# Kernel optimization log

Hardware: AMD Instinct MI355X
Metric: run time of the kernel (lower is better)

Reference implementation:

```python
import jax, jax.numpy as jnp
import numpy as np

B, T, E = 2, 2048, 1024
H = 16            # num_heads (global in source repo)
D = E // H        # head_len
LN_EPS = 1e-5


def setup_inputs() -> dict:
    key = jax.random.key(0)
    ks = jax.random.split(key, 12)
    s = lambda fan_in: 1.0 / np.sqrt(fan_in)
    return {
        "x":     jax.random.normal(ks[0], (B, T, E), jnp.float32),
        "ln1_g": jnp.ones((E,), jnp.float32),
        "ln1_b": jnp.zeros((E,), jnp.float32),
        "Wq":    jax.random.normal(ks[1], (E, E), jnp.float32) * s(E),
        "Wk":    jax.random.normal(ks[2], (E, E), jnp.float32) * s(E),
        "Wv":    jax.random.normal(ks[3], (E, E), jnp.float32) * s(E),
        "Wo":    jax.random.normal(ks[4], (E, E), jnp.float32) * s(E),
        "bo":    jnp.zeros((E,), jnp.float32),
        "ln2_g": jnp.ones((E,), jnp.float32),
        "ln2_b": jnp.zeros((E,), jnp.float32),
        "W1":    jax.random.normal(ks[5], (E, 4 * E), jnp.float32) * s(E),
        "b1":    jnp.zeros((4 * E,), jnp.float32),
        "W2":    jax.random.normal(ks[6], (4 * E, E), jnp.float32) * s(4 * E),
        "b2":    jnp.zeros((E,), jnp.float32),
    }


def _layernorm(x, g, b):
    mu = jnp.mean(x, axis=-1, keepdims=True)
    var = jnp.mean(jnp.square(x - mu), axis=-1, keepdims=True)
    return (x - mu) * jax.lax.rsqrt(var + LN_EPS) * g + b


def _attention(x, Wq, Wk, Wv, Wo, bo):
    b, t, e = x.shape
    q = (x @ Wq).reshape(b, t, H, D)
    k = (x @ Wk).reshape(b, t, H, D)
    v = (x @ Wv).reshape(b, t, H, D)
    scores = jnp.einsum("bqhd,bkhd->bhqk", q, k) / np.sqrt(D).astype(np.float32)
    causal = jnp.tril(jnp.ones((t, t), bool))
    scores = jnp.where(causal, scores, -jnp.inf)
    attn = jax.nn.softmax(scores, axis=-1)
    out = jnp.einsum("bhqk,bkhd->bqhd", attn, v).reshape(b, t, e)
    return out @ Wo + bo


def reference(x, ln1_g, ln1_b, Wq, Wk, Wv, Wo, bo, ln2_g, ln2_b, W1, b1, W2, b2):
    # pre-norm attention + residual (dropout=0 / eval mode)
    x = x + _attention(_layernorm(x, ln1_g, ln1_b), Wq, Wk, Wv, Wo, bo)
    # pre-norm MLP + residual
    h = _layernorm(x, ln2_g, ln2_b)
    h = jax.nn.relu(h @ W1 + b1) @ W2 + b2
    return x + h
```

## Files before the change

kernel.cpp:

```cpp
#include <hip/hip_runtime.h>
#include <cmath>
#include <cstdint>
#include <cstddef>

typedef __bf16 bf16_t;
typedef __bf16 bf16x8 __attribute__((ext_vector_type(8)));
typedef float  f32x4  __attribute__((ext_vector_type(4)));

#define B_   2
#define T_   2048
#define E_   1024
#define H_   16
#define D_   64
#define FF_  4096
#define NROW (B_ * T_)
#define QS_  (3 * E_)
#define NTI  (T_ / 64)

__global__ __launch_bounds__(256) void ln_kernel(
    const float* __restrict__ x, const float* __restrict__ g,
    const float* __restrict__ bta, bf16_t* __restrict__ out)
{
    int row = blockIdx.x;
    int tid = threadIdx.x;
    const float4* xr = (const float4*)(x + (size_t)row * E_);
    float4 v = xr[tid];
    float s  = v.x + v.y + v.z + v.w;
    float ss = v.x * v.x + v.y * v.y + v.z * v.z + v.w * v.w;
#pragma unroll
    for (int off = 32; off; off >>= 1) {
        s  += __shfl_xor(s, off);
        ss += __shfl_xor(ss, off);
    }
    __shared__ float red[8];
    int wave = tid >> 6, lane = tid & 63;
    if (lane == 0) { red[wave] = s; red[4 + wave] = ss; }
    __syncthreads();
    s  = red[0] + red[1] + red[2] + red[3];
    ss = red[4] + red[5] + red[6] + red[7];
    float mu   = s * (1.0f / E_);
    float var  = ss * (1.0f / E_) - mu * mu;
    float rstd = rsqrtf(var + 1e-5f);
    float4 gv = ((const float4*)g)[tid];
    float4 bv = ((const float4*)bta)[tid];
    union { bf16_t h[4]; ushort4 u; } pk;
    pk.h[0] = (bf16_t)((v.x - mu) * rstd * gv.x + bv.x);
    pk.h[1] = (bf16_t)((v.y - mu) * rstd * gv.y + bv.y);
    pk.h[2] = (bf16_t)((v.z - mu) * rstd * gv.z + bv.z);
    pk.h[3] = (bf16_t)((v.w - mu) * rstd * gv.w + bv.w);
    ((ushort4*)(out + (size_t)row * E_))[tid] = pk.u;
}

__global__ __launch_bounds__(256) void ln_reduce2(
    const float* __restrict__ p, const float* __restrict__ bias,
    const float* __restrict__ resid, float* __restrict__ x1,
    const float* __restrict__ g, const float* __restrict__ bta,
    bf16_t* __restrict__ out)
{
    int row = blockIdx.x;
    int tid = threadIdx.x;
    size_t off = (size_t)row * E_;
    float4 v0 = ((const float4*)(p + off))[tid];
    float4 v1 = ((const float4*)(p + (size_t)NROW * E_ + off))[tid];
    float4 bb = ((const float4*)bias)[tid];
    float4 rr = ((const float4*)(resid + off))[tid];
    float4 v;
    v.x = v0.x + v1.x + bb.x + rr.x;
    v.y = v0.y + v1.y + bb.y + rr.y;
    v.z = v0.z + v1.z + bb.z + rr.z;
    v.w = v0.w + v1.w + bb.w + rr.w;
    ((float4*)(x1 + off))[tid] = v;
    float s  = v.x + v.y + v.z + v.w;
    float ss = v.x * v.x + v.y * v.y + v.z * v.z + v.w * v.w;
#pragma unroll
    for (int o = 32; o; o >>= 1) {
        s  += __shfl_xor(s, o);
        ss += __shfl_xor(ss, o);
    }
    __shared__ float red[8];
    int wave = tid >> 6, lane = tid & 63;
    if (lane == 0) { red[wave] = s; red[4 + wave] = ss; }
    __syncthreads();
    s  = red[0] + red[1] + red[2] + red[3];
    ss = red[4] + red[5] + red[6] + red[7];
    float mu   = s * (1.0f / E_);
    float var  = ss * (1.0f / E_) - mu * mu;
    float rstd = rsqrtf(var + 1e-5f);
    float4 gv = ((const float4*)g)[tid];
    float4 bv = ((const float4*)bta)[tid];
    union { bf16_t h[4]; ushort4 u; } pk;
    pk.h[0] = (bf16_t)((v.x - mu) * rstd * gv.x + bv.x);
    pk.h[1] = (bf16_t)((v.y - mu) * rstd * gv.y + bv.y);
    pk.h[2] = (bf16_t)((v.z - mu) * rstd * gv.z + bv.z);
    pk.h[3] = (bf16_t)((v.w - mu) * rstd * gv.w + bv.w);
    ((ushort4*)(out + off))[tid] = pk.u;
}

__global__ __launch_bounds__(256) void add_reduce2(
    const float* __restrict__ p, const float* __restrict__ bias,
    const float* __restrict__ resid, float* __restrict__ out)
{
    int row = blockIdx.x;
    int tid = threadIdx.x;
    size_t off = (size_t)row * E_;
    float4 v0 = ((const float4*)(p + off))[tid];
    float4 v1 = ((const float4*)(p + (size_t)NROW * E_ + off))[tid];
    float4 bb = ((const float4*)bias)[tid];
    float4 rr = ((const float4*)(resid + off))[tid];
    float4 v;
    v.x = v0.x + v1.x + bb.x + rr.x;
    v.y = v0.y + v1.y + bb.y + rr.y;
    v.z = v0.z + v1.z + bb.z + rr.z;
    v.w = v0.w + v1.w + bb.w + rr.w;
    ((float4*)(out + off))[tid] = v;
}

__global__ __launch_bounds__(256) void transpose_all(
    const float* __restrict__ Wq, const float* __restrict__ Wk,
    const float* __restrict__ Wv, const float* __restrict__ Wo,
    const float* __restrict__ W1, const float* __restrict__ W2,
    bf16_t* __restrict__ wqkv, bf16_t* __restrict__ wot,
    bf16_t* __restrict__ w1t, bf16_t* __restrict__ w2t)
{
    int l = blockIdx.x;
    const float* W; bf16_t* Wt; int K, N, bx, by;
    if (l < 4096) {
        int seg = l >> 10, r = l & 1023;
        K = E_; N = E_; bx = r & 31; by = r >> 5;
        if      (seg == 0) { W = Wq; Wt = wqkv; }
        else if (seg == 1) { W = Wk; Wt = wqkv + (size_t)E_ * E_; }
        else if (seg == 2) { W = Wv; Wt = wqkv + (size_t)2 * E_ * E_; }
        else               { W = Wo; Wt = wot; }
    } else if (l < 8192) {
        int r = l - 4096; K = E_; N = FF_; bx = r & 127; by = r >> 7;
        W = W1; Wt = w1t;
    } else {
        int r = l - 8192; K = FF_; N = E_; bx = r & 31; by = r >> 5;
        W = W2; Wt = w2t;
    }
    __shared__ float t[32][33];
    int n0 = bx * 32, k0 = by * 32;
    int tx = threadIdx.x & 31, ty = threadIdx.x >> 5;
#pragma unroll
    for (int i = 0; i < 4; ++i)
        t[ty + i * 8][tx] = W[(size_t)(k0 + ty + i * 8) * N + n0 + tx];
    __syncthreads();
#pragma unroll
    for (int i = 0; i < 4; ++i)
        Wt[(size_t)(n0 + ty + i * 8) * K + k0 + tx] = (bf16_t)t[tx][ty + i * 8];
}

#define BM 128
#define BN 128
#define BK 32

__global__ __launch_bounds__(256) void gemm_bt(
    const bf16_t* __restrict__ A, const bf16_t* __restrict__ Bt,
    const float* __restrict__ bias, const float* __restrict__ resid,
    void* __restrict__ Cout, bf16_t* __restrict__ vt_out,
    int M, int N, int K, int lda, int ldb,
    int has_bias, int do_relu, int has_resid, int out_bf16)
{
    __shared__ __attribute__((aligned(16))) bf16_t As[2][BM * BK];
    __shared__ __attribute__((aligned(16))) bf16_t Bs[2][BN * BK];
    int tid  = threadIdx.x;
    int lane = tid & 63, wave = tid >> 6;
    int m0 = blockIdx.x * BM, n0 = blockIdx.y * BN;
    int wm = (wave & 1) * 64, wn = (wave >> 1) * 64;
    int koff = blockIdx.z * K;
    f32x4 acc[4][4];
#pragma unroll
    for (int i = 0; i < 4; ++i)
#pragma unroll
        for (int j = 0; j < 4; ++j) acc[i][j] = (f32x4){0.f, 0.f, 0.f, 0.f};

    int sr = tid >> 2;
    int sc = (tid & 3) * 8;
    const int kq = (lane >> 4) * 8;
    const int ml = lane & 15;
    const bf16_t* Ag = A  + (size_t)(m0 + sr) * lda + koff + sc;
    const bf16_t* Bg = Bt + (size_t)(n0 + sr) * ldb + koff + sc;
    int niter = K / BK;

    {
        uint4 ra0 = *(const uint4*)Ag;
        uint4 ra1 = *(const uint4*)(Ag + (size_t)64 * lda);
        uint4 rb0 = *(const uint4*)Bg;
        uint4 rb1 = *(const uint4*)(Bg + (size_t)64 * ldb);
        *(uint4*)&As[0][sr * BK + sc]        = ra0;
        *(uint4*)&As[0][(sr + 64) * BK + sc] = ra1;
        *(uint4*)&Bs[0][sr * BK + sc]        = rb0;
        *(uint4*)&Bs[0][(sr + 64) * BK + sc] = rb1;
    }

    for (int it = 0; it < niter; ++it) {
        int cur = it & 1, nxt = cur ^ 1;
        __syncthreads();

        uint4 ra0, ra1, rb0, rb1;
        bool pf = (it + 1 < niter);
        if (pf) {
            int k0 = (it + 1) * BK;
            ra0 = *(const uint4*)(Ag + k0);
            ra1 = *(const uint4*)(Ag + k0 + (size_t)64 * lda);
            rb0 = *(const uint4*)(Bg + k0);
            rb1 = *(const uint4*)(Bg + k0 + (size_t)64 * ldb);
        }

        bf16x8 af[4], bfr[4];
#pragma unroll
        for (int mi = 0; mi < 4; ++mi)
            af[mi] = *(const bf16x8*)&As[cur][(wm + mi * 16 + ml) * BK + kq];
#pragma unroll
        for (int ni = 0; ni < 4; ++ni)
            bfr[ni] = *(const bf16x8*)&Bs[cur][(wn + ni * 16 + ml) * BK + kq];
#pragma unroll
        for (int mi = 0; mi < 4; ++mi)
#pragma unroll
            for (int ni = 0; ni < 4; ++ni)
                acc[mi][ni] = __builtin_amdgcn_mfma_f32_16x16x32_bf16(
                    af[mi], bfr[ni], acc[mi][ni], 0, 0, 0);

        if (pf) {
            *(uint4*)&As[nxt][sr * BK + sc]        = ra0;
            *(uint4*)&As[nxt][(sr + 64) * BK + sc] = ra1;
            *(uint4*)&Bs[nxt][sr * BK + sc]        = rb0;
            *(uint4*)&Bs[nxt][(sr + 64) * BK + sc] = rb1;
        }
    }

    int r4 = (lane >> 4) * 4;
    if (gridDim.z > 1) {
        float* P = (float*)Cout + (size_t)blockIdx.z * M * N;
#pragma unroll
        for (int mi = 0; mi < 4; ++mi)
#pragma unroll
            for (int ni = 0; ni < 4; ++ni) {
                int col = n0 + wn + ni * 16 + ml;
#pragma unroll
                for (int r = 0; r < 4; ++r) {
                    int row = m0 + wm + mi * 16 + r4 + r;
                    P[(size_t)row * N + col] = acc[mi][ni][r];
                }
            }
        return;
    }
    if (vt_out && n0 >= 2 * E_) {
#pragma unroll
        for (int mi = 0; mi < 4; ++mi)
#pragma unroll
            for (int ni = 0; ni < 4; ++ni) {
                int vcol = n0 + wn + ni * 16 + ml - 2 * E_;
                int h = vcol >> 6, d = vcol & 63;
                int row0 = m0 + wm + mi * 16 + r4;
                int b = row0 >> 11, t = row0 & (T_ - 1);
                union { bf16_t h4[4]; uint2 u; } pk;
#pragma unroll
                for (int r = 0; r < 4; ++r) pk.h4[r] = (bf16_t)acc[mi][ni][r];
                *(uint2*)&vt_out[((size_t)(b * H_ + h) * D_ + d) * T_ + t] = pk.u;
            }
        return;
    }
#pragma unroll
    for (int mi = 0; mi < 4; ++mi) {
#pragma unroll
        for (int ni = 0; ni < 4; ++ni) {
            int col = n0 + wn + ni * 16 + ml;
            float bval = has_bias ? bias[col] : 0.0f;
#pragma unroll
            for (int r = 0; r < 4; ++r) {
                int row = m0 + wm + mi * 16 + r4 + r;
                float v = acc[mi][ni][r] + bval;
                if (do_relu)   v = fmaxf(v, 0.0f);
                if (has_resid) v += resid[(size_t)row * N + col];
                if (out_bf16)
                    ((bf16_t*)Cout)[(size_t)row * N + col] = (bf16_t)v;
                else
                    ((float*)Cout)[(size_t)row * N + col] = v;
            }
        }
    }
}

#define PSTR 72

struct TileState {
    f32x4 acc[4];
    float m1, l1;
};

__device__ __forceinline__ void tile_update(
    const bf16x8 kf[2][4], const bf16x8 vf[2][4], const bf16x8 qf[2],
    TileState& st, bf16_t* PsW, int ml, int r4, int kq8,
    bool diag, int ch, int qrow)
{
    f32x4 s[4];
#pragma unroll
    for (int nt = 0; nt < 4; ++nt) {
        s[nt] = (f32x4){0.f, 0.f, 0.f, 0.f};
#pragma unroll
        for (int ks = 0; ks < 2; ++ks)
            s[nt] = __builtin_amdgcn_mfma_f32_16x16x32_bf16(kf[ks][nt], qf[ks], s[nt], 0, 0, 0);
    }
    if (diag) {
#pragma unroll
        for (int nt = 0; nt < 4; ++nt)
#pragma unroll
            for (int r = 0; r < 4; ++r)
                if (ch * 64 + nt * 16 + r4 + r > qrow) s[nt][r] = -INFINITY;
    }
    float mx = -INFINITY;
#pragma unroll
    for (int nt = 0; nt < 4; ++nt)
#pragma unroll
        for (int r = 0; r < 4; ++r) mx = fmaxf(mx, s[nt][r]);
    mx = fmaxf(mx, __shfl_xor(mx, 16));
    mx = fmaxf(mx, __shfl_xor(mx, 32));
    float mn = fmaxf(st.m1, mx);
    float al = __expf(st.m1 - mn);
    st.m1 = mn;
    float sum = 0.f;
#pragma unroll
    for (int nt = 0; nt < 4; ++nt)
#pragma unroll
        for (int r = 0; r < 4; ++r) {
            float p = __expf(s[nt][r] - mn);
            s[nt][r] = p;
            sum += p;
        }
    sum += __shfl_xor(sum, 16);
    sum += __shfl_xor(sum, 32);
    st.l1 = st.l1 * al + sum;
#pragma unroll
    for (int dt = 0; dt < 4; ++dt)
#pragma unroll
        for (int r = 0; r < 4; ++r) st.acc[dt][r] *= al;

#pragma unroll
    for (int nt = 0; nt < 4; ++nt) {
        union { bf16_t h[4]; uint2 u; } pk;
#pragma unroll
        for (int r = 0; r < 4; ++r) pk.h[r] = (bf16_t)s[nt][r];
        *(uint2*)&PsW[ml * PSTR + nt * 16 + r4] = pk.u;
    }
#pragma unroll
    for (int ks = 0; ks < 2; ++ks) {
        bf16x8 pf = *(const bf16x8*)&PsW[ml * PSTR + ks * 32 + kq8];
#pragma unroll
        for (int dt = 0; dt < 4; ++dt)
            st.acc[dt] = __builtin_amdgcn_mfma_f32_16x16x32_bf16(vf[ks][dt], pf, st.acc[dt], 0, 0, 0);
    }
}

__global__ __launch_bounds__(256) void attn_mfma(
    const bf16_t* __restrict__ Qp, const bf16_t* __restrict__ Kp,
    const bf16_t* __restrict__ Vt, bf16_t* __restrict__ O)
{
    __shared__ __attribute__((aligned(16))) bf16_t Ks[2][64 * PSTR];
    __shared__ __attribute__((aligned(16))) bf16_t Vts[2][64 * PSTR];
    __shared__ __attribute__((aligned(16))) bf16_t Ps[4][16 * PSTR];

    int tid = threadIdx.x, lane = tid & 63, wave = tid >> 6;
    int ml  = lane & 15;
    int kq8 = (lane >> 4) * 8;
    int r4  = (lane >> 4) * 4;
    int bh = blockIdx.y, b = bh >> 4, h = bh & 15;
    size_t qk_base = (size_t)b * T_ * QS_ + h * D_;
    size_t vt_base = (size_t)bh * D_ * T_;
    size_t o_base  = (size_t)b * T_ * E_ + h * D_;

    int lo = blockIdx.x, hi = NTI - 1 - blockIdx.x;
    int qlo = lo * 64 + wave * 16;
    int qhi = hi * 64 + wave * 16;

    bf16x8 qfl[2], qfh[2];
#pragma unroll
    for (int ks = 0; ks < 2; ++ks) {
        bf16x8 a = *(const bf16x8*)&Qp[qk_base + (size_t)(qlo + ml) * QS_ + ks * 32 + kq8];
        bf16x8 c = *(const bf16x8*)&Qp[qk_base + (size_t)(qhi + ml) * QS_ + ks * 32 + kq8];
#pragma unroll
        for (int j = 0; j < 8; ++j) {
            a[j] = (bf16_t)((float)a[j] * 0.125f);
            c[j] = (bf16_t)((float)c[j] * 0.125f);
        }
        qfl[ks] = a; qfh[ks] = c;
    }

    TileState stl, sth;
#pragma unroll
    for (int dt = 0; dt < 4; ++dt) {
        stl.acc[dt] = (f32x4){0.f, 0.f, 0.f, 0.f};
        sth.acc[dt] = (f32x4){0.f, 0.f, 0.f, 0.f};
    }
    stl.m1 = -INFINITY; stl.l1 = 0.f;
    sth.m1 = -INFINITY; sth.l1 = 0.f;

    int r0 = tid >> 3, c0 = (tid & 7) * 8;
    int nch = hi + 1;

    {
        const bf16_t* kb = &Kp[qk_base + (size_t)r0 * QS_ + c0];
        const bf16_t* vb = &Vt[vt_base + (size_t)r0 * T_ + c0];
        uint4 k0v = *(const uint4*)kb;
        uint4 k1v = *(const uint4*)(kb + (size_t)32 * QS_);
        uint4 v0v = *(const uint4*)vb;
        uint4 v1v = *(const uint4*)(vb + (size_t)32 * T_);
        *(uint4*)&Ks[0][r0 * PSTR + c0]         = k0v;
        *(uint4*)&Ks[0][(r0 + 32) * PSTR + c0]  = k1v;
        *(uint4*)&Vts[0][r0 * PSTR + c0]        = v0v;
        *(uint4*)&Vts[0][(r0 + 32) * PSTR + c0] = v1v;
    }

    for (int ch = 0; ch < nch; ++ch) {
        int cur = ch & 1, nxt = cur ^ 1;
        __syncthreads();

        uint4 nk0, nk1, nv0, nv1;
        bool pf = (ch + 1 < nch);
        if (pf) {
            const bf16_t* kb = &Kp[qk_base + (size_t)((ch + 1) * 64 + r0) * QS_ + c0];
            const bf16_t* vb = &Vt[vt_base + (size_t)r0 * T_ + (ch + 1) * 64 + c0];
            nk0 = *(const uint4*)kb;
            nk1 = *(const uint4*)(kb + (size_t)32 * QS_);
            nv0 = *(const uint4*)vb;
            nv1 = *(const uint4*)(vb + (size_t)32 * T_);
        }

        bf16x8 kf[2][4], vf[2][4];
#pragma unroll
        for (int ks = 0; ks < 2; ++ks)
#pragma unroll
            for (int nt = 0; nt < 4; ++nt) {
                kf[ks][nt] = *(const bf16x8*)&Ks[cur][(nt * 16 + ml) * PSTR + ks * 32 + kq8];
                vf[ks][nt] = *(const bf16x8*)&Vts[cur][(nt * 16 + ml) * PSTR + ks * 32 + kq8];
            }

        tile_update(kf, vf, qfh, sth, Ps[wave], ml, r4, kq8,
                    ch == hi, ch, qhi + ml);
        if (ch <= lo)
            tile_update(kf, vf, qfl, stl, Ps[wave], ml, r4, kq8,
                        ch == lo, ch, qlo + ml);

        if (pf) {
            *(uint4*)&Ks[nxt][r0 * PSTR + c0]         = nk0;
            *(uint4*)&Ks[nxt][(r0 + 32) * PSTR + c0]  = nk1;
            *(uint4*)&Vts[nxt][r0 * PSTR + c0]        = nv0;
            *(uint4*)&Vts[nxt][(r0 + 32) * PSTR + c0] = nv1;
        }
    }

#pragma unroll
    for (int t = 0; t < 2; ++t) {
        TileState& st = t ? stl : sth;
        int qw = t ? qlo : qhi;
        float inv = 1.0f / st.l1;
#pragma unroll
        for (int dt = 0; dt < 4; ++dt) {
            union { bf16_t h[4]; uint2 u; } pk;
#pragma unroll
            for (int r = 0; r < 4; ++r) pk.h[r] = (bf16_t)(st.acc[dt][r] * inv);
            *(uint2*)&Ps[wave][ml * PSTR + dt * 16 + r4] = pk.u;
        }
        int row = lane >> 2, seg = (lane & 3) * 16;
        bf16x8 o0 = *(const bf16x8*)&Ps[wave][row * PSTR + seg];
        bf16x8 o1 = *(const bf16x8*)&Ps[wave][row * PSTR + seg + 8];
        size_t gp = o_base + (size_t)(qw + row) * E_ + seg;
        *(bf16x8*)&O[gp]     = o0;
        *(bf16x8*)&O[gp + 8] = o1;
    }
}

extern "C" void kernel_launch(void* const* d_in, const int* in_sizes, int n_in,
                              void* d_out, int out_size, void* d_ws, size_t ws_size,
                              hipStream_t stream)
{
    const float* x    = (const float*)d_in[0];
    const float* ln1g = (const float*)d_in[1];
    const float* ln1b = (const float*)d_in[2];
    const float* Wq   = (const float*)d_in[3];
    const float* Wk   = (const float*)d_in[4];
    const float* Wv   = (const float*)d_in[5];
    const float* Wo   = (const float*)d_in[6];
    const float* bo   = (const float*)d_in[7];
    const float* ln2g = (const float*)d_in[8];
    const float* ln2b = (const float*)d_in[9];
    const float* W1   = (const float*)d_in[10];
    const float* b1   = (const float*)d_in[11];
    const float* W2   = (const float*)d_in[12];
    const float* b2   = (const float*)d_in[13];

    char* ws = (char*)d_ws;
    const size_t MB = 1024ull * 1024ull;
    bf16_t* wqkv = (bf16_t*)(ws + 0 * MB);
    bf16_t* wot  = (bf16_t*)(ws + 6 * MB);
    bf16_t* w1t  = (bf16_t*)(ws + 8 * MB);
    bf16_t* w2t  = (bf16_t*)(ws + 16 * MB);
    bf16_t* xn   = (bf16_t*)(ws + 24 * MB);
    bf16_t* QKV  = (bf16_t*)(ws + 32 * MB);
    bf16_t* att  = (bf16_t*)(ws + 56 * MB);
    float*  x1   = (float*)(ws + 64 * MB);
    bf16_t* hb   = (bf16_t*)(ws + 80 * MB);
    bf16_t* h1   = (bf16_t*)(ws + 88 * MB);
    bf16_t* Vtb  = (bf16_t*)(ws + 88 * MB);
    float*  part = (float*)(ws + 24 * MB);

    dim3 blk(256);

    transpose_all<<<dim3(12288), blk, 0, stream>>>(
        Wq, Wk, Wv, Wo, W1, W2, wqkv, wot, w1t, w2t);

    ln_kernel<<<dim3(NROW), blk, 0, stream>>>(x, ln1g, ln1b, xn);

    gemm_bt<<<dim3(NROW / BM, QS_ / BN), blk, 0, stream>>>(
        xn, wqkv, nullptr, nullptr, QKV, Vtb, NROW, QS_, E_, E_, E_, 0, 0, 0, 1);

    attn_mfma<<<dim3(NTI / 2, B_ * H_), blk, 0, stream>>>(
        QKV, QKV + E_, Vtb, att);

    gemm_bt<<<dim3(NROW / BM, E_ / BN, 2), blk, 0, stream>>>(
        att, wot, nullptr, nullptr, part, nullptr, NROW, E_, E_ / 2, E_, E_, 0, 0, 0, 0);
    ln_reduce2<<<dim3(NROW), blk, 0, stream>>>(
        part, bo, x, x1, ln2g, ln2b, hb);

    gemm_bt<<<dim3(NROW / BM, FF_ / BN), blk, 0, stream>>>(
        hb, w1t, b1, nullptr, h1, nullptr, NROW, FF_, E_, E_, E_, 1, 1, 0, 1);

    gemm_bt<<<dim3(NROW / BM, E_ / BN, 2), blk, 0, stream>>>(
        h1, w2t, nullptr, nullptr, part, nullptr, NROW, E_, FF_ / 2, FF_, FF_, 0, 0, 0, 0);
    add_reduce2<<<dim3(NROW), blk, 0, stream>>>(
        part, b2, x1, (float*)d_out);
}
```

Measured before the change: 342.6 us.

## Deepen GEMM global prefetch to two tiles and use lightweight LDS barrier

Rewrites the gemm_bt main loop into a manually unrolled two-stage loop that keeps two register prefetch sets in flight, so global loads for tile k+2 are issued while tile k is being computed. It also replaces __syncthreads with an inline s_waitcnt lgkmcnt(0) plus s_barrier, which skips waiting on outstanding global loads at the barrier. The aim is to hide more global memory latency behind MFMA work. The extra prefetch registers raise register pressure, and the hand-written barrier relies on only LDS operations needing ordering at that point.

```diff
diff --git a/kernel.cpp b/kernel.cpp
--- a/kernel.cpp
+++ b/kernel.cpp
@@ -16,6 +16,10 @@
 #define NROW (B_ * T_)
 #define QS_  (3 * E_)
 #define NTI  (T_ / 64)
+
+__device__ __forceinline__ void wg_barrier() {
+    asm volatile("s_waitcnt lgkmcnt(0)\n\ts_barrier" ::: "memory");
+}
 
 __global__ __launch_bounds__(256) void ln_kernel(
     const float* __restrict__ x, const float* __restrict__ g,
@@ -154,6 +158,47 @@
 #define BN 128
 #define BK 32
 
+struct Pref { uint4 a0, a1, b0, b1; };
+
+__device__ __forceinline__ Pref ld_tile(
+    const bf16_t* Ag, const bf16_t* Bg, int k0, int lda, int ldb)
+{
+    Pref p;
+    p.a0 = *(const uint4*)(Ag + k0);
+    p.a1 = *(const uint4*)(Ag + k0 + (size_t)64 * lda);
+    p.b0 = *(const uint4*)(Bg + k0);
+    p.b1 = *(const uint4*)(Bg + k0 + (size_t)64 * ldb);
+    return p;
+}
+
+__device__ __forceinline__ void st_tile(
+    bf16_t* As, bf16_t* Bs, int sr, int sc, const Pref& p)
+{
+    *(uint4*)&As[sr * BK + sc]        = p.a0;
+    *(uint4*)&As[(sr + 64) * BK + sc] = p.a1;
+    *(uint4*)&Bs[sr * BK + sc]        = p.b0;
+    *(uint4*)&Bs[(sr + 64) * BK + sc] = p.b1;
+}
+
+__device__ __forceinline__ void mfma_tile(
+    const bf16_t* As, const bf16_t* Bs, f32x4 acc[4][4],
+    int wm, int wn, int ml, int kq)
+{
+    bf16x8 af[4], bfr[4];
+#pragma unroll
+    for (int mi = 0; mi < 4; ++mi)
+        af[mi] = *(const bf16x8*)&As[(wm + mi * 16 + ml) * BK + kq];
+#pragma unroll
+    for (int ni = 0; ni < 4; ++ni)
+        bfr[ni] = *(const bf16x8*)&Bs[(wn + ni * 16 + ml) * BK + kq];
+#pragma unroll
+    for (int mi = 0; mi < 4; ++mi)
+#pragma unroll
+        for (int ni = 0; ni < 4; ++ni)
+            acc[mi][ni] = __builtin_amdgcn_mfma_f32_16x16x32_bf16(
+                af[mi], bfr[ni], acc[mi][ni], 0, 0, 0);
+}
+
 __global__ __launch_bounds__(256) void gemm_bt(
     const bf16_t* __restrict__ A, const bf16_t* __restrict__ Bt,
     const float* __restrict__ bias, const float* __restrict__ resid,
@@ -182,51 +227,23 @@
     const bf16_t* Bg = Bt + (size_t)(n0 + sr) * ldb + koff + sc;
     int niter = K / BK;
 
-    {
-        uint4 ra0 = *(const uint4*)Ag;
-        uint4 ra1 = *(const uint4*)(Ag + (size_t)64 * lda);
-        uint4 rb0 = *(const uint4*)Bg;
-        uint4 rb1 = *(const uint4*)(Bg + (size_t)64 * ldb);
-        *(uint4*)&As[0][sr * BK + sc]        = ra0;
-        *(uint4*)&As[0][(sr + 64) * BK + sc] = ra1;
-        *(uint4*)&Bs[0][sr * BK + sc]        = rb0;
-        *(uint4*)&Bs[0][(sr + 64) * BK + sc] = rb1;
-    }
-
-    for (int it = 0; it < niter; ++it) {
-        int cur = it & 1, nxt = cur ^ 1;
-        __syncthreads();
-
-        uint4 ra0, ra1, rb0, rb1;
-        bool pf = (it + 1 < niter);
-        if (pf) {
-            int k0 = (it + 1) * BK;
-            ra0 = *(const uint4*)(Ag + k0);
-            ra1 = *(const uint4*)(Ag + k0 + (size_t)64 * lda);
-            rb0 = *(const uint4*)(Bg + k0);
-            rb1 = *(const uint4*)(Bg + k0 + (size_t)64 * ldb);
-        }
-
-        bf16x8 af[4], bfr[4];
-#pragma unroll
-        for (int mi = 0; mi < 4; ++mi)
-            af[mi] = *(const bf16x8*)&As[cur][(wm + mi * 16 + ml) * BK + kq];
-#pragma unroll
-        for (int ni = 0; ni < 4; ++ni)
-            bfr[ni] = *(const bf16x8*)&Bs[cur][(wn + ni * 16 + ml) * BK + kq];
-#pragma unroll
-        for (int mi = 0; mi < 4; ++mi)
-#pragma unroll
-            for (int ni = 0; ni < 4; ++ni)
-                acc[mi][ni] = __builtin_amdgcn_mfma_f32_16x16x32_bf16(
-                    af[mi], bfr[ni], acc[mi][ni], 0, 0, 0);
-
-        if (pf) {
-            *(uint4*)&As[nxt][sr * BK + sc]        = ra0;
-            *(uint4*)&As[nxt][(sr + 64) * BK + sc] = ra1;
-            *(uint4*)&Bs[nxt][sr * BK + sc]        = rb0;
-            *(uint4*)&Bs[nxt][(sr + 64) * BK + sc] = rb1;
-        }
+    Pref pA, pB;
+    st_tile(As[0], Bs[0], sr, sc, ld_tile(Ag, Bg, 0, lda, ldb));
+    if (niter > 1) pB = ld_tile(Ag, Bg, BK, lda, ldb);
+
+    for (int it = 0; it < niter; it += 2) {
+        wg_barrier();
+        bool pfA = (it + 2 < niter);
+        if (pfA) pA = ld_tile(Ag, Bg, (it + 2) * BK, lda, ldb);
+        mfma_tile(As[0], Bs[0], acc, wm, wn, ml, kq);
+        if (it + 1 < niter) st_tile(As[1], Bs[1], sr, sc, pB);
+        if (it + 1 >= niter) break;
+
+        wg_barrier();
+        bool pfB = (it + 3 < niter);
+        if (pfB) pB = ld_tile(Ag, Bg, (it + 3) * BK, lda, ldb);
+        mfma_tile(As[1], Bs[1], acc, wm, wn, ml, kq);
+        if (pfA) st_tile(As[0], Bs[0], sr, sc, pA);
     }
 
     int r4 = (lane >> 4) * 4;
```

Result: slower. 466.0 us (+36.0%).
